# Performance work log

Measured on AMD Instinct MI355X. Metric: run time of the kernel, lower is better.

Reference implementation:

```python
import jax, jax.numpy as jnp
import numpy as np

B, T, L_CTX = 64, 150, 256
H = 512   # decoder_num_hidden
E = 512   # target_embedding_size
V = 1000  # target_vocab_size


def setup_inputs() -> dict:
    key = jax.random.key(0)
    ks = jax.random.split(key, 10)
    s = 0.05
    return {
        "cnn_feats": jax.random.normal(ks[0], (B, L_CTX, H), dtype=jnp.float32),
        "seq": jax.random.randint(ks[1], (B, T), 0, V, dtype=jnp.int32),
        "embed_table": jax.random.normal(ks[2], (V, E), dtype=jnp.float32) * s,
        "W_ih": jax.random.normal(ks[3], (4 * H, E), dtype=jnp.float32) * s,
        "b_ih": jnp.zeros((4 * H,), dtype=jnp.float32),
        "W_hh": jax.random.normal(ks[4], (4 * H, H), dtype=jnp.float32) * s,
        "b_hh": jnp.zeros((4 * H,), dtype=jnp.float32),
        "W_hm": jax.random.normal(ks[5], (H, H), dtype=jnp.float32) * s,
        "W_om": jax.random.normal(ks[6], (H, 2 * H), dtype=jnp.float32) * s,
        "W_logit": jax.random.normal(ks[7], (V, H), dtype=jnp.float32) * s,
        "b_logit": jnp.zeros((V,), dtype=jnp.float32),
    }


def reference(cnn_feats, seq, embed_table, W_ih, b_ih, W_hh, b_hh,
              W_hm, W_om, W_logit, b_logit):
    # Single-layer LSTMCell decoder with per-step attention (eval mode, dropout=0).
    def step(carry, it):
        h, c = carry                      # [B,H] each
        xt = jax.nn.relu(embed_table[it])  # [B,E]
        gates = xt @ W_ih.T + b_ih + h @ W_hh.T + b_hh  # [B,4H]
        i, f, g, o = jnp.split(gates, 4, axis=1)
        c2 = jax.nn.sigmoid(f) * c + jax.nn.sigmoid(i) * jnp.tanh(g)
        h2 = jax.nn.sigmoid(o) * jnp.tanh(c2)
        mapped = h2 @ W_hm.T              # [B,H]
        attn = jnp.einsum("blh,bh->bl", cnn_feats, mapped)
        w = jax.nn.softmax(attn, axis=1)
        ctx = jnp.einsum("bl,blh->bh", w, cnn_feats)
        out = jnp.concatenate([ctx, h2], axis=1) @ W_om.T  # [B,H]
        logp = jax.nn.log_softmax(out @ W_logit.T + b_logit, axis=1)
        return (h2, c2), logp

    bsz = cnn_feats.shape[0]
    h0 = jnp.zeros((bsz, W_hh.shape[1]), dtype=cnn_feats.dtype)
    c0 = jnp.zeros_like(h0)
    _, outs = jax.lax.scan(step, (h0, c0), seq.T)  # outs: [T,B,V]
    return outs.transpose(1, 0, 2)  # [B,T,V]
```

## Files before the change

kernel.cpp:

```cpp
#include <hip/hip_runtime.h>
#include <math.h>

#define B_  64
#define T_  150
#define L_  256
#define H_  512
#define E_  512
#define V_  1000
#define G4_ 2048
#define DB_ 16
#define HCB 32

typedef _Float16 f16;
typedef f16   f16x8 __attribute__((ext_vector_type(8)));
typedef f16   f16x4 __attribute__((ext_vector_type(4)));
typedef float f32x4 __attribute__((ext_vector_type(4)));
typedef unsigned long long ull;

__device__ __forceinline__ float sigmf(float x) { return 1.0f / (1.0f + expf(-x)); }

__global__ __launch_bounds__(512) void decoder_mfma(
    const int*   __restrict__ seq,
    const float* __restrict__ G,
    const float* __restrict__ Whh,
    ull*  __restrict__ xh,
    int*  __restrict__ tags,
    float* __restrict__ hbuf)
{
    __shared__ f16   hlds[64][520];
    __shared__ float glds[64][132];
    __shared__ float csh[64][36];

    const int tid = threadIdx.x;
    const int bb  = blockIdx.x;
    const int ln  = tid & 63;
    const int wv  = tid >> 6;
    const int mh  = wv >> 2;
    const int nt2 = wv & 3;

    f16x8 bfr[2][16];
    #pragma unroll
    for (int j = 0; j < 2; ++j) {
        const int n = 2 * nt2 + j;
        const int grow = (n >> 1) * H_ + bb * HCB + (n & 1) * 16 + (ln & 15);
        #pragma unroll
        for (int kt = 0; kt < 16; ++kt) {
            const int k0 = kt * 32 + (ln >> 4) * 8;
            float4 w0 = *(const float4*)(Whh + (size_t)grow * H_ + k0);
            float4 w1 = *(const float4*)(Whh + (size_t)grow * H_ + k0 + 4);
            bfr[j][kt] = (f16x8){(f16)w0.x, (f16)w0.y, (f16)w0.z, (f16)w0.w,
                                 (f16)w1.x, (f16)w1.y, (f16)w1.z, (f16)w1.w};
        }
    }
    for (int e = tid; e < 64 * 520 / 4; e += 512) ((ull*)hlds)[e] = 0ull;
    for (int e = tid; e < 64 * 36; e += 512) ((float*)csh)[e] = 0.f;
    __syncthreads();

    const int cb = tid >> 3, cg = tid & 7;

    for (int t = 0; t < T_; ++t) {
        const int v = seq[cb * T_ + t];
        const float* gp = G + (size_t)v * G4_ + bb * HCB + cg * 4;
        float4 gq0 = *(const float4*)(gp);
        float4 gq1 = *(const float4*)(gp + H_);
        float4 gq2 = *(const float4*)(gp + 2 * H_);
        float4 gq3 = *(const float4*)(gp + 3 * H_);

        if (t > 0) {
            if (tid < DB_) {
                while (__hip_atomic_load(&tags[tid], __ATOMIC_RELAXED,
                                         __HIP_MEMORY_SCOPE_AGENT) < t) {}
            }
            __syncthreads();
            const ull* src = xh + (size_t)(t & 1) * 64 * 128;
            ull v0[8], v1[8];
            #pragma unroll
            for (int it = 0; it < 8; ++it) {
                const int e = tid + it * 512;
                const int b = e >> 6, s = e & 63;
                v0[it] = __hip_atomic_load(&src[b * 128 + 2 * s], __ATOMIC_RELAXED,
                                           __HIP_MEMORY_SCOPE_AGENT);
                v1[it] = __hip_atomic_load(&src[b * 128 + 2 * s + 1], __ATOMIC_RELAXED,
                                           __HIP_MEMORY_SCOPE_AGENT);
            }
            #pragma unroll
            for (int it = 0; it < 8; ++it) {
                const int e = tid + it * 512;
                const int b = e >> 6, s = e & 63;
                ull* dst = (ull*)&hlds[b][s * 8];
                dst[0] = v0[it]; dst[1] = v1[it];
            }
            __syncthreads();
        }

        f32x4 acc00 = {0.f,0.f,0.f,0.f}, acc01 = {0.f,0.f,0.f,0.f};
        f32x4 acc10 = {0.f,0.f,0.f,0.f}, acc11 = {0.f,0.f,0.f,0.f};
        #pragma unroll
        for (int kt = 0; kt < 16; ++kt) {
            const int ko = kt * 32 + (ln >> 4) * 8;
            f16x8 a0 = *(const f16x8*)&hlds[(2 * mh)     * 16 + (ln & 15)][ko];
            f16x8 a1 = *(const f16x8*)&hlds[(2 * mh + 1) * 16 + (ln & 15)][ko];
            acc00 = __builtin_amdgcn_mfma_f32_16x16x32_f16(a0, bfr[0][kt], acc00, 0, 0, 0);
            acc01 = __builtin_amdgcn_mfma_f32_16x16x32_f16(a0, bfr[1][kt], acc01, 0, 0, 0);
            acc10 = __builtin_amdgcn_mfma_f32_16x16x32_f16(a1, bfr[0][kt], acc10, 0, 0, 0);
            acc11 = __builtin_amdgcn_mfma_f32_16x16x32_f16(a1, bfr[1][kt], acc11, 0, 0, 0);
        }
        {
            const int r0 = (2 * mh) * 16 + (ln >> 4) * 4;
            const int r1 = (2 * mh + 1) * 16 + (ln >> 4) * 4;
            const int c0 = (2 * nt2) * 16 + (ln & 15);
            const int c1 = (2 * nt2 + 1) * 16 + (ln & 15);
            #pragma unroll
            for (int i = 0; i < 4; ++i) {
                glds[r0 + i][c0] = acc00[i];
                glds[r0 + i][c1] = acc01[i];
                glds[r1 + i][c0] = acc10[i];
                glds[r1 + i][c1] = acc11[i];
            }
        }
        __syncthreads();

        {
            float4 Gi = *(const float4*)&glds[cb][cg * 4];
            float4 Gf = *(const float4*)&glds[cb][32 + cg * 4];
            float4 Gg = *(const float4*)&glds[cb][64 + cg * 4];
            float4 Go = *(const float4*)&glds[cb][96 + cg * 4];
            float4 cold = *(const float4*)&csh[cb][cg * 4];
            float gi[4] = {Gi.x + gq0.x, Gi.y + gq0.y, Gi.z + gq0.z, Gi.w + gq0.w};
            float gf[4] = {Gf.x + gq1.x, Gf.y + gq1.y, Gf.z + gq1.z, Gf.w + gq1.w};
            float gg[4] = {Gg.x + gq2.x, Gg.y + gq2.y, Gg.z + gq2.z, Gg.w + gq2.w};
            float go[4] = {Go.x + gq3.x, Go.y + gq3.y, Go.z + gq3.z, Go.w + gq3.w};
            float cl[4] = {cold.x, cold.y, cold.z, cold.w};
            float4 cnew, hnew;
            f16x4 hp;
            #pragma unroll
            for (int i = 0; i < 4; ++i) {
                float c2 = sigmf(gf[i]) * cl[i] + sigmf(gi[i]) * tanhf(gg[i]);
                float h2 = sigmf(go[i]) * tanhf(c2);
                ((float*)&cnew)[i] = c2;
                ((float*)&hnew)[i] = h2;
                hp[i] = (f16)h2;
            }
            *(float4*)&csh[cb][cg * 4] = cnew;
            *(float4*)&hbuf[((size_t)t * 64 + cb) * H_ + bb * HCB + cg * 4] = hnew;
            __hip_atomic_store(
                &xh[(size_t)((t + 1) & 1) * 64 * 128 + cb * 128 + bb * 8 + cg],
                __builtin_bit_cast(ull, hp),
                __ATOMIC_RELAXED, __HIP_MEMORY_SCOPE_AGENT);
        }
        __syncthreads();
        if (tid == 0)
            __hip_atomic_store(&tags[bb], t + 1, __ATOMIC_RELAXED,
                               __HIP_MEMORY_SCOPE_AGENT);
    }
}

template<bool RELU_A, bool REMAP>
__global__ __launch_bounds__(256) void gemm16_nt(
    const float* __restrict__ A1, const float* __restrict__ A2,
    const float* __restrict__ Bm,
    const float* __restrict__ bias1, const float* __restrict__ bias2,
    float* __restrict__ C, int M, int N, int KA)
{
    __shared__ f16 As[64][40];
    __shared__ f16 Bs[64][40];
    const int tid = threadIdx.x;
    const int m0 = blockIdx.x * 64, n0 = blockIdx.y * 64;
    const int ln = tid & 63, wv = tid >> 6;
    const int lr = tid >> 2, lc8 = (tid & 3) * 8;
    const int K = A2 ? 2 * KA : KA;
    f32x4 acc[4] = {};

    for (int kb = 0; kb < K; kb += 32) {
        const float* Ap; int kk;
        if (kb < KA) { Ap = A1; kk = kb; } else { Ap = A2; kk = kb - KA; }
        int gm = m0 + lr;
        float4 a0 = make_float4(0.f, 0.f, 0.f, 0.f), a1 = a0;
        if (gm < M) {
            a0 = *(const float4*)(Ap + (size_t)gm * KA + kk + lc8);
            a1 = *(const float4*)(Ap + (size_t)gm * KA + kk + lc8 + 4);
        }
        if (RELU_A) {
            a0.x = fmaxf(a0.x, 0.f); a0.y = fmaxf(a0.y, 0.f);
            a0.z = fmaxf(a0.z, 0.f); a0.w = fmaxf(a0.w, 0.f);
            a1.x = fmaxf(a1.x, 0.f); a1.y = fmaxf(a1.y, 0.f);
            a1.z = fmaxf(a1.z, 0.f); a1.w = fmaxf(a1.w, 0.f);
        }
        f16x8 av = {(f16)a0.x, (f16)a0.y, (f16)a0.z, (f16)a0.w,
                    (f16)a1.x, (f16)a1.y, (f16)a1.z, (f16)a1.w};
        *(f16x8*)&As[lr][lc8] = av;

        int gn = n0 + lr;
        float4 b0 = make_float4(0.f, 0.f, 0.f, 0.f), b1 = b0;
        if (gn < N) {
            b0 = *(const float4*)(Bm + (size_t)gn * K + kb + lc8);
            b1 = *(const float4*)(Bm + (size_t)gn * K + kb + lc8 + 4);
        }
        f16x8 bv = {(f16)b0.x, (f16)b0.y, (f16)b0.z, (f16)b0.w,
                    (f16)b1.x, (f16)b1.y, (f16)b1.z, (f16)b1.w};
        *(f16x8*)&Bs[lr][lc8] = bv;
        __syncthreads();

        f16x8 af = *(const f16x8*)&As[wv * 16 + (ln & 15)][(ln >> 4) * 8];
        #pragma unroll
        for (int ntt = 0; ntt < 4; ++ntt) {
            f16x8 bf = *(const f16x8*)&Bs[ntt * 16 + (ln & 15)][(ln >> 4) * 8];
            acc[ntt] = __builtin_amdgcn_mfma_f32_16x16x32_f16(af, bf, acc[ntt], 0, 0, 0);
        }
        __syncthreads();
    }

    #pragma unroll
    for (int ntt = 0; ntt < 4; ++ntt) {
        #pragma unroll
        for (int i = 0; i < 4; ++i) {
            int gm = m0 + wv * 16 + (ln >> 4) * 4 + i;
            int gn = n0 + ntt * 16 + (ln & 15);
            if (gm < M && gn < N) {
                float v = acc[ntt][i];
                if (bias1) v += bias1[gn];
                if (bias2) v += bias2[gn];
                size_t row = REMAP ? ((size_t)(gm & 63) * T_ + (gm >> 6)) : (size_t)gm;
                C[row * (size_t)N + gn] = v;
            }
        }
    }
}

__global__ __launch_bounds__(256) void gemm_nt(
    const float* __restrict__ A, size_t lda, size_t azs,
    const float* __restrict__ Bm, size_t ldb, size_t bzs,
    float* __restrict__ C, size_t ldc, size_t czs, int M, int N, int K)
{
    A  += blockIdx.z * azs;
    Bm += blockIdx.z * bzs;
    C  += blockIdx.z * czs;
    __shared__ __align__(16) float As[16][68];
    __shared__ __align__(16) float Bs[16][68];
    const int tid = threadIdx.x;
    const int m0 = blockIdx.x * 64;
    const int n0 = blockIdx.y * 64;
    const int lr = tid >> 2;
    const int lc = (tid & 3) << 2;
    const int tm = (tid & 15) << 2;
    const int tn = (tid >> 4) << 2;
    float acc[4][4] = {};

    for (int kb = 0; kb < K; kb += 16) {
        float4 a4 = make_float4(0.f, 0.f, 0.f, 0.f);
        int gm = m0 + lr;
        if (gm < M) a4 = *(const float4*)(A + (size_t)gm * lda + kb + lc);
        As[lc + 0][lr] = a4.x; As[lc + 1][lr] = a4.y;
        As[lc + 2][lr] = a4.z; As[lc + 3][lr] = a4.w;

        float4 b4 = make_float4(0.f, 0.f, 0.f, 0.f);
        int gn = n0 + lr;
        if (gn < N) b4 = *(const float4*)(Bm + (size_t)gn * ldb + kb + lc);
        Bs[lc + 0][lr] = b4.x; Bs[lc + 1][lr] = b4.y;
        Bs[lc + 2][lr] = b4.z; Bs[lc + 3][lr] = b4.w;
        __syncthreads();

        #pragma unroll
        for (int k = 0; k < 16; ++k) {
            float4 av = *(const float4*)&As[k][tm];
            float4 bv = *(const float4*)&Bs[k][tn];
            float af[4] = {av.x, av.y, av.z, av.w};
            float bf[4] = {bv.x, bv.y, bv.z, bv.w};
            #pragma unroll
            for (int i = 0; i < 4; ++i)
                #pragma unroll
                for (int j = 0; j < 4; ++j)
                    acc[i][j] += af[i] * bf[j];
        }
        __syncthreads();
    }

    #pragma unroll
    for (int i = 0; i < 4; ++i) {
        int gm = m0 + tm + i;
        if (gm >= M) continue;
        #pragma unroll
        for (int j = 0; j < 4; ++j) {
            int gn = n0 + tn + j;
            if (gn >= N) continue;
            C[(size_t)gm * ldc + gn] = acc[i][j];
        }
    }
}

__global__ __launch_bounds__(256) void gemm_nn(
    const float* __restrict__ A, size_t lda, size_t azs,
    const float* __restrict__ Bm, size_t ldb, size_t bzs,
    float* __restrict__ C, size_t ldc, size_t czs, int M, int N, int K)
{
    A  += blockIdx.z * azs;
    Bm += blockIdx.z * bzs;
    C  += blockIdx.z * czs;
    __shared__ __align__(16) float As[16][68];
    __shared__ __align__(16) float Bs[16][68];
    const int tid = threadIdx.x;
    const int m0 = blockIdx.x * 64;
    const int n0 = blockIdx.y * 64;
    const int lr = tid >> 2;
    const int lc = (tid & 3) << 2;
    const int br = tid >> 4;
    const int bc = (tid & 15) << 2;
    const int tm = (tid & 15) << 2;
    const int tn = (tid >> 4) << 2;
    float acc[4][4] = {};

    for (int kb = 0; kb < K; kb += 16) {
        float4 a4 = make_float4(0.f, 0.f, 0.f, 0.f);
        int gm = m0 + lr;
        if (gm < M) a4 = *(const float4*)(A + (size_t)gm * lda + kb + lc);
        As[lc + 0][lr] = a4.x; As[lc + 1][lr] = a4.y;
        As[lc + 2][lr] = a4.z; As[lc + 3][lr] = a4.w;

        float4 b4 = make_float4(0.f, 0.f, 0.f, 0.f);
        if (n0 + bc < N) b4 = *(const float4*)(Bm + (size_t)(kb + br) * ldb + n0 + bc);
        Bs[br][bc + 0] = b4.x; Bs[br][bc + 1] = b4.y;
        Bs[br][bc + 2] = b4.z; Bs[br][bc + 3] = b4.w;
        __syncthreads();

        #pragma unroll
        for (int k = 0; k < 16; ++k) {
            float4 av = *(const float4*)&As[k][tm];
            float4 bv = *(const float4*)&Bs[k][tn];
            float af[4] = {av.x, av.y, av.z, av.w};
            float bf[4] = {bv.x, bv.y, bv.z, bv.w};
            #pragma unroll
            for (int i = 0; i < 4; ++i)
                #pragma unroll
                for (int j = 0; j < 4; ++j)
                    acc[i][j] += af[i] * bf[j];
        }
        __syncthreads();
    }

    #pragma unroll
    for (int i = 0; i < 4; ++i) {
        int gm = m0 + tm + i;
        if (gm >= M) continue;
        #pragma unroll
        for (int j = 0; j < 4; ++j) {
            int gn = n0 + tn + j;
            if (gn >= N) continue;
            C[(size_t)gm * ldc + gn] = acc[i][j];
        }
    }
}

__global__ __launch_bounds__(256) void att_softmax(float* __restrict__ att, int nrows)
{
    const int tid = threadIdx.x, lane = tid & 63, wave = tid >> 6;
    const int row = blockIdx.x * 4 + wave;
    if (row >= nrows) return;
    float4* p = (float4*)(att + (size_t)row * L_);
    float4 sc = p[lane];
    float mx = fmaxf(fmaxf(sc.x, sc.y), fmaxf(sc.z, sc.w));
    #pragma unroll
    for (int off = 32; off; off >>= 1) mx = fmaxf(mx, __shfl_xor(mx, off));
    float e0 = expf(sc.x - mx), e1 = expf(sc.y - mx);
    float e2 = expf(sc.z - mx), e3 = expf(sc.w - mx);
    float s = e0 + e1 + e2 + e3;
    #pragma unroll
    for (int off = 32; off; off >>= 1) s += __shfl_xor(s, off);
    float inv = 1.f / s;
    p[lane] = make_float4(e0 * inv, e1 * inv, e2 * inv, e3 * inv);
}

__global__ __launch_bounds__(256) void logsoftmax_k(float* __restrict__ out)
{
    const int row = blockIdx.x;
    float* p = out + (size_t)row * V_;
    const int tid = threadIdx.x, lane = tid & 63, wave = tid >> 6;
    __shared__ float red[8];

    float vals[4];
    int n = 0;
    float mx = -INFINITY;
    for (int v = tid; v < V_; v += 256) { vals[n] = p[v]; mx = fmaxf(mx, vals[n]); ++n; }
    #pragma unroll
    for (int off = 32; off; off >>= 1) mx = fmaxf(mx, __shfl_xor(mx, off));
    if (lane == 0) red[wave] = mx;
    __syncthreads();
    mx = fmaxf(fmaxf(red[0], red[1]), fmaxf(red[2], red[3]));

    float s = 0.f;
    for (int i = 0; i < n; ++i) s += expf(vals[i] - mx);
    #pragma unroll
    for (int off = 32; off; off >>= 1) s += __shfl_xor(s, off);
    if (lane == 0) red[4 + wave] = s;
    __syncthreads();
    s = red[4] + red[5] + red[6] + red[7];

    const float lse = mx + logf(s);
    n = 0;
    for (int v = tid; v < V_; v += 256) { p[v] = vals[n] - lse; ++n; }
}

extern "C" void kernel_launch(void* const* d_in, const int* in_sizes, int n_in,
                              void* d_out, int out_size, void* d_ws, size_t ws_size,
                              hipStream_t stream)
{
    const float* cnn     = (const float*)d_in[0];
    const int*   seq     = (const int*)d_in[1];
    const float* embed   = (const float*)d_in[2];
    const float* W_ih    = (const float*)d_in[3];
    const float* b_ih    = (const float*)d_in[4];
    const float* W_hh    = (const float*)d_in[5];
    const float* b_hh    = (const float*)d_in[6];
    const float* W_hm    = (const float*)d_in[7];
    const float* W_om    = (const float*)d_in[8];
    const float* W_logit = (const float*)d_in[9];
    const float* b_logit = (const float*)d_in[10];
    float* out = (float*)d_out;

    float* ws = (float*)d_ws;
    float* G    = ws;
    float* hbuf = G + (size_t)V_ * G4_;
    float* outv = hbuf + (size_t)B_ * T_ * H_;
    ull*   xh   = (ull*)(outv + (size_t)B_ * T_ * H_);
    int*   tags = (int*)(xh + 2 * 64 * 128);
    float* mapped = out;
    float* attb   = out + (size_t)B_ * T_ * H_;

    hipMemsetAsync(tags, 0, DB_ * sizeof(int), stream);

    gemm16_nt<true, false><<<dim3(16, 32), 256, 0, stream>>>(
        embed, nullptr, W_ih, b_ih, b_hh, G, V_, G4_, E_);

    decoder_mfma<<<DB_, 512, 0, stream>>>(seq, G, W_hh, xh, tags, hbuf);

    gemm16_nt<false, false><<<dim3(150, 8), 256, 0, stream>>>(
        hbuf, nullptr, W_hm, nullptr, nullptr, mapped, B_ * T_, H_, H_);
    gemm_nt<<<dim3(3, 4, 64), 256, 0, stream>>>(
        mapped, (size_t)B_ * H_, H_,
        cnn, H_, (size_t)L_ * H_,
        attb, L_, (size_t)T_ * L_, T_, L_, H_);
    att_softmax<<<(B_ * T_ + 3) / 4, 256, 0, stream>>>(attb, B_ * T_);
    gemm_nn<<<dim3(3, 8, 64), 256, 0, stream>>>(
        attb, L_, (size_t)T_ * L_,
        cnn, H_, (size_t)L_ * H_,
        mapped, (size_t)B_ * H_, H_, T_, H_, L_);
    gemm16_nt<false, false><<<dim3(150, 8), 256, 0, stream>>>(
        mapped, hbuf, W_om, nullptr, nullptr, outv, B_ * T_, H_, H_);
    gemm16_nt<false, true><<<dim3(150, 16), 256, 0, stream>>>(
        outv, nullptr, W_logit, b_logit, nullptr, out, B_ * T_, V_, H_);
    logsoftmax_k<<<B_ * T_, 256, 0, stream>>>(out);
}
```

Measured before the change: 1.078 ms.

## Fuse attention and output head into decoder kernel with consumer blocks overlapping recurrence

Launches 64 extra consumer blocks alongside the 16 recurrence blocks. Each consumer block waits on the per-step tags, reads 16 steps of h history for its batch row and computes the mapping, attention scores, softmax, context, output projection, logits and log-softmax in fp16 MFMA. This overlaps the post-recurrence work with the sequential LSTM and removes several separate GEMM and softmax launches along with the fp32 intermediate buffers. It adds pre-cast fp16 weight and transposed-feature kernels plus a full h history buffer, and it depends on all 80 blocks being co-resident to avoid deadlock.

```diff
diff --git a/kernel.cpp b/kernel.cpp
--- a/kernel.cpp
+++ b/kernel.cpp
@@ -19,60 +19,68 @@
 
 __device__ __forceinline__ float sigmf(float x) { return 1.0f / (1.0f + expf(-x)); }
 
-__global__ __launch_bounds__(512) void decoder_mfma(
+__global__ __launch_bounds__(512) void fused_decoder(
     const int*   __restrict__ seq,
     const float* __restrict__ G,
     const float* __restrict__ Whh,
-    ull*  __restrict__ xh,
+    const float* __restrict__ cnn,
+    const f16*   __restrict__ Vt16,
+    const f16*   __restrict__ Whm16,
+    const f16*   __restrict__ Wom16,
+    const f16*   __restrict__ Wlogit16,
+    const float* __restrict__ b_logit,
+    ull*  __restrict__ xhist,
     int*  __restrict__ tags,
-    float* __restrict__ hbuf)
+    float* __restrict__ out)
 {
-    __shared__ f16   hlds[64][520];
-    __shared__ float glds[64][132];
-    __shared__ float csh[64][36];
+    __shared__ __align__(16) char smem[140800];
 
     const int tid = threadIdx.x;
-    const int bb  = blockIdx.x;
+    const int bx  = blockIdx.x;
     const int ln  = tid & 63;
     const int wv  = tid >> 6;
-    const int mh  = wv >> 2;
-    const int nt2 = wv & 3;
-
-    f16x8 bfr[2][16];
-    #pragma unroll
-    for (int j = 0; j < 2; ++j) {
-        const int n = 2 * nt2 + j;
-        const int grow = (n >> 1) * H_ + bb * HCB + (n & 1) * 16 + (ln & 15);
+
+    if (bx < DB_) {
+        f16   (*hlds)[520] = (f16(*)[520])smem;
+        float (*glds)[132] = (float(*)[132])(smem + 66560);
+        float (*csh)[36]   = (float(*)[36])(smem + 100352);
+        const int bb  = bx;
+        const int mh  = wv >> 2;
+        const int nt2 = wv & 3;
+
+        f16x8 bfr[2][16];
         #pragma unroll
-        for (int kt = 0; kt < 16; ++kt) {
-            const int k0 = kt * 32 + (ln >> 4) * 8;
-            float4 w0 = *(const float4*)(Whh + (size_t)grow * H_ + k0);
-            float4 w1 = *(const float4*)(Whh + (size_t)grow * H_ + k0 + 4);
-            bfr[j][kt] = (f16x8){(f16)w0.x, (f16)w0.y, (f16)w0.z, (f16)w0.w,
-                                 (f16)w1.x, (f16)w1.y, (f16)w1.z, (f16)w1.w};
-        }
-    }
-    for (int e = tid; e < 64 * 520 / 4; e += 512) ((ull*)hlds)[e] = 0ull;
-    for (int e = tid; e < 64 * 36; e += 512) ((float*)csh)[e] = 0.f;
-    __syncthreads();
-
-    const int cb = tid >> 3, cg = tid & 7;
-
-    for (int t = 0; t < T_; ++t) {
-        const int v = seq[cb * T_ + t];
-        const float* gp = G + (size_t)v * G4_ + bb * HCB + cg * 4;
-        float4 gq0 = *(const float4*)(gp);
-        float4 gq1 = *(const float4*)(gp + H_);
-        float4 gq2 = *(const float4*)(gp + 2 * H_);
-        float4 gq3 = *(const float4*)(gp + 3 * H_);
-
-        if (t > 0) {
+        for (int j = 0; j < 2; ++j) {
+            const int n = 2 * nt2 + j;
+            const int grow = (n >> 1) * H_ + bb * HCB + (n & 1) * 16 + (ln & 15);
+            #pragma unroll
+            for (int kt = 0; kt < 16; ++kt) {
+                const int k0 = kt * 32 + (ln >> 4) * 8;
+                float4 w0 = *(const float4*)(Whh + (size_t)grow * H_ + k0);
+                float4 w1 = *(const float4*)(Whh + (size_t)grow * H_ + k0 + 4);
+                bfr[j][kt] = (f16x8){(f16)w0.x, (f16)w0.y, (f16)w0.z, (f16)w0.w,
+                                     (f16)w1.x, (f16)w1.y, (f16)w1.z, (f16)w1.w};
+            }
+        }
+        for (int e = tid; e < 64 * 36; e += 512) ((float*)csh)[e] = 0.f;
+        __syncthreads();
+
+        const int cb = tid >> 3, cg = tid & 7;
+
+        for (int t = 0; t < T_; ++t) {
+            const int v = seq[cb * T_ + t];
+            const float* gp = G + (size_t)v * G4_ + bb * HCB + cg * 4;
+            float4 gq0 = *(const float4*)(gp);
+            float4 gq1 = *(const float4*)(gp + H_);
+            float4 gq2 = *(const float4*)(gp + 2 * H_);
+            float4 gq3 = *(const float4*)(gp + 3 * H_);
+
             if (tid < DB_) {
                 while (__hip_atomic_load(&tags[tid], __ATOMIC_RELAXED,
                                          __HIP_MEMORY_SCOPE_AGENT) < t) {}
             }
             __syncthreads();
-            const ull* src = xh + (size_t)(t & 1) * 64 * 128;
+            const ull* src = xhist + (size_t)t * 8192;
             ull v0[8], v1[8];
             #pragma unroll
             for (int it = 0; it < 8; ++it) {
@@ -91,76 +99,240 @@
                 dst[0] = v0[it]; dst[1] = v1[it];
             }
             __syncthreads();
-        }
-
-        f32x4 acc00 = {0.f,0.f,0.f,0.f}, acc01 = {0.f,0.f,0.f,0.f};
-        f32x4 acc10 = {0.f,0.f,0.f,0.f}, acc11 = {0.f,0.f,0.f,0.f};
-        #pragma unroll
-        for (int kt = 0; kt < 16; ++kt) {
-            const int ko = kt * 32 + (ln >> 4) * 8;
-            f16x8 a0 = *(const f16x8*)&hlds[(2 * mh)     * 16 + (ln & 15)][ko];
-            f16x8 a1 = *(const f16x8*)&hlds[(2 * mh + 1) * 16 + (ln & 15)][ko];
-            acc00 = __builtin_amdgcn_mfma_f32_16x16x32_f16(a0, bfr[0][kt], acc00, 0, 0, 0);
-            acc01 = __builtin_amdgcn_mfma_f32_16x16x32_f16(a0, bfr[1][kt], acc01, 0, 0, 0);
-            acc10 = __builtin_amdgcn_mfma_f32_16x16x32_f16(a1, bfr[0][kt], acc10, 0, 0, 0);
-            acc11 = __builtin_amdgcn_mfma_f32_16x16x32_f16(a1, bfr[1][kt], acc11, 0, 0, 0);
-        }
-        {
-            const int r0 = (2 * mh) * 16 + (ln >> 4) * 4;
-            const int r1 = (2 * mh + 1) * 16 + (ln >> 4) * 4;
-            const int c0 = (2 * nt2) * 16 + (ln & 15);
-            const int c1 = (2 * nt2 + 1) * 16 + (ln & 15);
-            #pragma unroll
-            for (int i = 0; i < 4; ++i) {
-                glds[r0 + i][c0] = acc00[i];
-                glds[r0 + i][c1] = acc01[i];
-                glds[r1 + i][c0] = acc10[i];
-                glds[r1 + i][c1] = acc11[i];
-            }
-        }
-        __syncthreads();
-
-        {
-            float4 Gi = *(const float4*)&glds[cb][cg * 4];
-            float4 Gf = *(const float4*)&glds[cb][32 + cg * 4];
-            float4 Gg = *(const float4*)&glds[cb][64 + cg * 4];
-            float4 Go = *(const float4*)&glds[cb][96 + cg * 4];
-            float4 cold = *(const float4*)&csh[cb][cg * 4];
-            float gi[4] = {Gi.x + gq0.x, Gi.y + gq0.y, Gi.z + gq0.z, Gi.w + gq0.w};
-            float gf[4] = {Gf.x + gq1.x, Gf.y + gq1.y, Gf.z + gq1.z, Gf.w + gq1.w};
-            float gg[4] = {Gg.x + gq2.x, Gg.y + gq2.y, Gg.z + gq2.z, Gg.w + gq2.w};
-            float go[4] = {Go.x + gq3.x, Go.y + gq3.y, Go.z + gq3.z, Go.w + gq3.w};
-            float cl[4] = {cold.x, cold.y, cold.z, cold.w};
-            float4 cnew, hnew;
-            f16x4 hp;
-            #pragma unroll
-            for (int i = 0; i < 4; ++i) {
-                float c2 = sigmf(gf[i]) * cl[i] + sigmf(gi[i]) * tanhf(gg[i]);
-                float h2 = sigmf(go[i]) * tanhf(c2);
-                ((float*)&cnew)[i] = c2;
-                ((float*)&hnew)[i] = h2;
-                hp[i] = (f16)h2;
-            }
-            *(float4*)&csh[cb][cg * 4] = cnew;
-            *(float4*)&hbuf[((size_t)t * 64 + cb) * H_ + bb * HCB + cg * 4] = hnew;
-            __hip_atomic_store(
-                &xh[(size_t)((t + 1) & 1) * 64 * 128 + cb * 128 + bb * 8 + cg],
-                __builtin_bit_cast(ull, hp),
-                __ATOMIC_RELAXED, __HIP_MEMORY_SCOPE_AGENT);
-        }
-        __syncthreads();
-        if (tid == 0)
-            __hip_atomic_store(&tags[bb], t + 1, __ATOMIC_RELAXED,
-                               __HIP_MEMORY_SCOPE_AGENT);
+
+            f32x4 acc00 = {0.f,0.f,0.f,0.f}, acc01 = {0.f,0.f,0.f,0.f};
+            f32x4 acc10 = {0.f,0.f,0.f,0.f}, acc11 = {0.f,0.f,0.f,0.f};
+            #pragma unroll
+            for (int kt = 0; kt < 16; ++kt) {
+                const int ko = kt * 32 + (ln >> 4) * 8;
+                f16x8 a0 = *(const f16x8*)&hlds[(2 * mh)     * 16 + (ln & 15)][ko];
+                f16x8 a1 = *(const f16x8*)&hlds[(2 * mh + 1) * 16 + (ln & 15)][ko];
+                acc00 = __builtin_amdgcn_mfma_f32_16x16x32_f16(a0, bfr[0][kt], acc00, 0, 0, 0);
+                acc01 = __builtin_amdgcn_mfma_f32_16x16x32_f16(a0, bfr[1][kt], acc01, 0, 0, 0);
+                acc10 = __builtin_amdgcn_mfma_f32_16x16x32_f16(a1, bfr[0][kt], acc10, 0, 0, 0);
+                acc11 = __builtin_amdgcn_mfma_f32_16x16x32_f16(a1, bfr[1][kt], acc11, 0, 0, 0);
+            }
+            {
+                const int r0 = (2 * mh) * 16 + (ln >> 4) * 4;
+                const int r1 = (2 * mh + 1) * 16 + (ln >> 4) * 4;
+                const int c0 = (2 * nt2) * 16 + (ln & 15);
+                const int c1 = (2 * nt2 + 1) * 16 + (ln & 15);
+                #pragma unroll
+                for (int i = 0; i < 4; ++i) {
+                    glds[r0 + i][c0] = acc00[i];
+                    glds[r0 + i][c1] = acc01[i];
+                    glds[r1 + i][c0] = acc10[i];
+                    glds[r1 + i][c1] = acc11[i];
+                }
+            }
+            __syncthreads();
+
+            {
+                float4 Gi = *(const float4*)&glds[cb][cg * 4];
+                float4 Gf = *(const float4*)&glds[cb][32 + cg * 4];
+                float4 Gg = *(const float4*)&glds[cb][64 + cg * 4];
+                float4 Go = *(const float4*)&glds[cb][96 + cg * 4];
+                float4 cold = *(const float4*)&csh[cb][cg * 4];
+                float gi[4] = {Gi.x + gq0.x, Gi.y + gq0.y, Gi.z + gq0.z, Gi.w + gq0.w};
+                float gf[4] = {Gf.x + gq1.x, Gf.y + gq1.y, Gf.z + gq1.z, Gf.w + gq1.w};
+                float gg[4] = {Gg.x + gq2.x, Gg.y + gq2.y, Gg.z + gq2.z, Gg.w + gq2.w};
+                float go[4] = {Go.x + gq3.x, Go.y + gq3.y, Go.z + gq3.z, Go.w + gq3.w};
+                float cl[4] = {cold.x, cold.y, cold.z, cold.w};
+                float4 cnew;
+                f16x4 hp;
+                #pragma unroll
+                for (int i = 0; i < 4; ++i) {
+                    float c2 = sigmf(gf[i]) * cl[i] + sigmf(gi[i]) * tanhf(gg[i]);
+                    float h2 = sigmf(go[i]) * tanhf(c2);
+                    ((float*)&cnew)[i] = c2;
+                    hp[i] = (f16)h2;
+                }
+                *(float4*)&csh[cb][cg * 4] = cnew;
+                __hip_atomic_store(
+                    &xhist[(size_t)(t + 1) * 8192 + cb * 128 + bb * 8 + cg],
+                    __builtin_bit_cast(ull, hp),
+                    __ATOMIC_RELAXED, __HIP_MEMORY_SCOPE_AGENT);
+            }
+            __syncthreads();
+            if (tid == 0)
+                __hip_atomic_store(&tags[bb], t + 1, __ATOMIC_RELAXED,
+                                   __HIP_MEMORY_SCOPE_AGENT);
+        }
+    } else {
+        const int b = bx - DB_;
+        f16   (*hl)[520]  = (f16(*)[520])smem;
+        f16   (*ml)[520]  = (f16(*)[520])(smem + 16640);
+        float (*sl)[260]  = (float(*)[260])(smem + 33280);
+        f16   (*pl)[264]  = (f16(*)[264])(smem + 49920);
+        f16   (*ol)[520]  = (f16(*)[520])(smem + 58368);
+        float (*ll)[1028] = (float(*)[1028])(smem + 75008);
+
+        const float* cnnb = cnn + (size_t)b * L_ * H_;
+        const f16*   vtb  = Vt16 + (size_t)b * H_ * L_;
+        const int ln15 = ln & 15;
+        const int ln4  = (ln >> 4) * 8;
+        const int lr4  = (ln >> 4) * 4;
+
+        for (int t0 = 0; t0 < T_; t0 += 16) {
+            const int NB = (T_ - t0 < 16) ? (T_ - t0) : 16;
+            if (tid < DB_) {
+                while (__hip_atomic_load(&tags[tid], __ATOMIC_RELAXED,
+                                         __HIP_MEMORY_SCOPE_AGENT) < t0 + NB)
+                    __builtin_amdgcn_s_sleep(8);
+            }
+            __syncthreads();
+            for (int e = tid; e < NB * 128; e += 512) {
+                int tt = e >> 7, s = e & 127;
+                ull v = __hip_atomic_load(
+                    &xhist[(size_t)(t0 + 1 + tt) * 8192 + b * 128 + s],
+                    __ATOMIC_RELAXED, __HIP_MEMORY_SCOPE_AGENT);
+                *(ull*)&hl[tt][s * 4] = v;
+            }
+            __syncthreads();
+
+            {
+                f32x4 acc[4] = {};
+                for (int kt = 0; kt < 16; ++kt) {
+                    f16x8 a = *(const f16x8*)&hl[ln15][kt * 32 + ln4];
+                    #pragma unroll
+                    for (int j = 0; j < 4; ++j) {
+                        int n = wv * 64 + j * 16 + ln15;
+                        f16x8 bf = *(const f16x8*)(Whm16 + (size_t)n * 512 + kt * 32 + ln4);
+                        acc[j] = __builtin_amdgcn_mfma_f32_16x16x32_f16(a, bf, acc[j], 0, 0, 0);
+                    }
+                }
+                #pragma unroll
+                for (int j = 0; j < 4; ++j)
+                    #pragma unroll
+                    for (int i = 0; i < 4; ++i)
+                        ml[lr4 + i][wv * 64 + j * 16 + ln15] = (f16)acc[j][i];
+            }
+            __syncthreads();
+            {
+                f32x4 acc[2] = {};
+                for (int kt = 0; kt < 16; ++kt) {
+                    f16x8 a = *(const f16x8*)&ml[ln15][kt * 32 + ln4];
+                    #pragma unroll
+                    for (int j = 0; j < 2; ++j) {
+                        int l = wv * 32 + j * 16 + ln15;
+                        float4 w0 = *(const float4*)(cnnb + (size_t)l * H_ + kt * 32 + ln4);
+                        float4 w1 = *(const float4*)(cnnb + (size_t)l * H_ + kt * 32 + ln4 + 4);
+                        f16x8 bf = {(f16)w0.x, (f16)w0.y, (f16)w0.z, (f16)w0.w,
+                                    (f16)w1.x, (f16)w1.y, (f16)w1.z, (f16)w1.w};
+                        acc[j] = __builtin_amdgcn_mfma_f32_16x16x32_f16(a, bf, acc[j], 0, 0, 0);
+                    }
+                }
+                #pragma unroll
+                for (int j = 0; j < 2; ++j)
+                    #pragma unroll
+                    for (int i = 0; i < 4; ++i)
+                        sl[lr4 + i][wv * 32 + j * 16 + ln15] = acc[j][i];
+            }
+            __syncthreads();
+            #pragma unroll
+            for (int rr = 0; rr < 2; ++rr) {
+                int r = wv * 2 + rr;
+                float4 v = *(const float4*)&sl[r][ln * 4];
+                float mx = fmaxf(fmaxf(v.x, v.y), fmaxf(v.z, v.w));
+                #pragma unroll
+                for (int off = 32; off; off >>= 1) mx = fmaxf(mx, __shfl_xor(mx, off));
+                float e0 = expf(v.x - mx), e1 = expf(v.y - mx);
+                float e2 = expf(v.z - mx), e3 = expf(v.w - mx);
+                float s = e0 + e1 + e2 + e3;
+                #pragma unroll
+                for (int off = 32; off; off >>= 1) s += __shfl_xor(s, off);
+                float inv = 1.f / s;
+                f16x4 p = {(f16)(e0 * inv), (f16)(e1 * inv), (f16)(e2 * inv), (f16)(e3 * inv)};
+                *(f16x4*)&pl[r][ln * 4] = p;
+            }
+            __syncthreads();
+            {
+                f32x4 acc[4] = {};
+                for (int kt = 0; kt < 8; ++kt) {
+                    f16x8 a = *(const f16x8*)&pl[ln15][kt * 32 + ln4];
+                    #pragma unroll
+                    for (int j = 0; j < 4; ++j) {
+                        int n = wv * 64 + j * 16 + ln15;
+                        f16x8 bf = *(const f16x8*)(vtb + (size_t)n * L_ + kt * 32 + ln4);
+                        acc[j] = __builtin_amdgcn_mfma_f32_16x16x32_f16(a, bf, acc[j], 0, 0, 0);
+                    }
+                }
+                __syncthreads();
+                #pragma unroll
+                for (int j = 0; j < 4; ++j)
+                    #pragma unroll
+                    for (int i = 0; i < 4; ++i)
+                        ml[lr4 + i][wv * 64 + j * 16 + ln15] = (f16)acc[j][i];
+            }
+            __syncthreads();
+            {
+                f32x4 acc[4] = {};
+                for (int kt = 0; kt < 32; ++kt) {
+                    f16x8 a = (kt < 16)
+                        ? *(const f16x8*)&ml[ln15][kt * 32 + ln4]
+                        : *(const f16x8*)&hl[ln15][(kt - 16) * 32 + ln4];
+                    #pragma unroll
+                    for (int j = 0; j < 4; ++j) {
+                        int n = wv * 64 + j * 16 + ln15;
+                        f16x8 bf = *(const f16x8*)(Wom16 + (size_t)n * 1024 + kt * 32 + ln4);
+                        acc[j] = __builtin_amdgcn_mfma_f32_16x16x32_f16(a, bf, acc[j], 0, 0, 0);
+                    }
+                }
+                #pragma unroll
+                for (int j = 0; j < 4; ++j)
+                    #pragma unroll
+                    for (int i = 0; i < 4; ++i)
+                        ol[lr4 + i][wv * 64 + j * 16 + ln15] = (f16)acc[j][i];
+            }
+            __syncthreads();
+            {
+                f32x4 acc[8] = {};
+                for (int kt = 0; kt < 16; ++kt) {
+                    f16x8 a = *(const f16x8*)&ol[ln15][kt * 32 + ln4];
+                    #pragma unroll
+                    for (int j = 0; j < 8; ++j) {
+                        int n = wv * 128 + j * 16 + ln15;
+                        f16x8 bf = *(const f16x8*)(Wlogit16 + (size_t)n * 512 + kt * 32 + ln4);
+                        acc[j] = __builtin_amdgcn_mfma_f32_16x16x32_f16(a, bf, acc[j], 0, 0, 0);
+                    }
+                }
+                #pragma unroll
+                for (int j = 0; j < 8; ++j) {
+                    int n = wv * 128 + j * 16 + ln15;
+                    float bias = (n < V_) ? b_logit[n] : 0.f;
+                    #pragma unroll
+                    for (int i = 0; i < 4; ++i)
+                        ll[lr4 + i][n] = acc[j][i] + bias;
+                }
+            }
+            __syncthreads();
+            #pragma unroll
+            for (int rr = 0; rr < 2; ++rr) {
+                int r = wv * 2 + rr;
+                if (r < NB) {
+                    float mx = -INFINITY;
+                    for (int i = ln; i < V_; i += 64) mx = fmaxf(mx, ll[r][i]);
+                    #pragma unroll
+                    for (int off = 32; off; off >>= 1) mx = fmaxf(mx, __shfl_xor(mx, off));
+                    float s = 0.f;
+                    for (int i = ln; i < V_; i += 64) s += expf(ll[r][i] - mx);
+                    #pragma unroll
+                    for (int off = 32; off; off >>= 1) s += __shfl_xor(s, off);
+                    float lse = mx + logf(s);
+                    float* dst = out + ((size_t)b * T_ + t0 + r) * V_;
+                    for (int i = ln; i < V_; i += 64) dst[i] = ll[r][i] - lse;
+                }
+            }
+            __syncthreads();
+        }
     }
 }
 
-template<bool RELU_A, bool REMAP>
+template<bool RELU_A>
 __global__ __launch_bounds__(256) void gemm16_nt(
-    const float* __restrict__ A1, const float* __restrict__ A2,
-    const float* __restrict__ Bm,
+    const float* __restrict__ A1, const float* __restrict__ Bm,
     const float* __restrict__ bias1, const float* __restrict__ bias2,
-    float* __restrict__ C, int M, int N, int KA)
+    float* __restrict__ C, int M, int N, int K)
 {
     __shared__ f16 As[64][40];
     __shared__ f16 Bs[64][40];
@@ -168,17 +340,14 @@
     const int m0 = blockIdx.x * 64, n0 = blockIdx.y * 64;
     const int ln = tid & 63, wv = tid >> 6;
     const int lr = tid >> 2, lc8 = (tid & 3) * 8;
-    const int K = A2 ? 2 * KA : KA;
     f32x4 acc[4] = {};
 
     for (int kb = 0; kb < K; kb += 32) {
-        const float* Ap; int kk;
-        if (kb < KA) { Ap = A1; kk = kb; } else { Ap = A2; kk = kb - KA; }
         int gm = m0 + lr;
         float4 a0 = make_float4(0.f, 0.f, 0.f, 0.f), a1 = a0;
         if (gm < M) {
-            a0 = *(const float4*)(Ap + (size_t)gm * KA + kk + lc8);
-            a1 = *(const float4*)(Ap + (size_t)gm * KA + kk + lc8 + 4);
+            a0 = *(const float4*)(A1 + (size_t)gm * K + kb + lc8);
+            a1 = *(const float4*)(A1 + (size_t)gm * K + kb + lc8 + 4);
         }
         if (RELU_A) {
             a0.x = fmaxf(a0.x, 0.f); a0.y = fmaxf(a0.y, 0.f);
@@ -211,7 +380,7 @@
     }
 
     #pragma unroll
-    for (int ntt = 0; ntt < 4; ++ntt) {
+    for (int ntt = 0; ntt < 4; ++ntt)
         #pragma unroll
         for (int i = 0; i < 4; ++i) {
             int gm = m0 + wv * 16 + (ln >> 4) * 4 + i;
@@ -220,183 +389,36 @@
                 float v = acc[ntt][i];
                 if (bias1) v += bias1[gn];
                 if (bias2) v += bias2[gn];
-                size_t row = REMAP ? ((size_t)(gm & 63) * T_ + (gm >> 6)) : (size_t)gm;
-                C[row * (size_t)N + gn] = v;
-            }
-        }
-    }
+                C[(size_t)gm * N + gn] = v;
+            }
+        }
 }
 
-__global__ __launch_bounds__(256) void gemm_nt(
-    const float* __restrict__ A, size_t lda, size_t azs,
-    const float* __restrict__ Bm, size_t ldb, size_t bzs,
-    float* __restrict__ C, size_t ldc, size_t czs, int M, int N, int K)
+__global__ __launch_bounds__(256) void wcast(
+    const float* __restrict__ whm, const float* __restrict__ wom,
+    const float* __restrict__ wlg,
+    f16* __restrict__ o_whm, f16* __restrict__ o_wom, f16* __restrict__ o_wlg)
 {
-    A  += blockIdx.z * azs;
-    Bm += blockIdx.z * bzs;
-    C  += blockIdx.z * czs;
-    __shared__ __align__(16) float As[16][68];
-    __shared__ __align__(16) float Bs[16][68];
-    const int tid = threadIdx.x;
-    const int m0 = blockIdx.x * 64;
-    const int n0 = blockIdx.y * 64;
-    const int lr = tid >> 2;
-    const int lc = (tid & 3) << 2;
-    const int tm = (tid & 15) << 2;
-    const int tn = (tid >> 4) << 2;
-    float acc[4][4] = {};
-
-    for (int kb = 0; kb < K; kb += 16) {
-        float4 a4 = make_float4(0.f, 0.f, 0.f, 0.f);
-        int gm = m0 + lr;
-        if (gm < M) a4 = *(const float4*)(A + (size_t)gm * lda + kb + lc);
-        As[lc + 0][lr] = a4.x; As[lc + 1][lr] = a4.y;
-        As[lc + 2][lr] = a4.z; As[lc + 3][lr] = a4.w;
-
-        float4 b4 = make_float4(0.f, 0.f, 0.f, 0.f);
-        int gn = n0 + lr;
-        if (gn < N) b4 = *(const float4*)(Bm + (size_t)gn * ldb + kb + lc);
-        Bs[lc + 0][lr] = b4.x; Bs[lc + 1][lr] = b4.y;
-        Bs[lc + 2][lr] = b4.z; Bs[lc + 3][lr] = b4.w;
-        __syncthreads();
-
-        #pragma unroll
-        for (int k = 0; k < 16; ++k) {
-            float4 av = *(const float4*)&As[k][tm];
-            float4 bv = *(const float4*)&Bs[k][tn];
-            float af[4] = {av.x, av.y, av.z, av.w};
-            float bf[4] = {bv.x, bv.y, bv.z, bv.w};
-            #pragma unroll
-            for (int i = 0; i < 4; ++i)
-                #pragma unroll
-                for (int j = 0; j < 4; ++j)
-                    acc[i][j] += af[i] * bf[j];
-        }
-        __syncthreads();
-    }
-
-    #pragma unroll
-    for (int i = 0; i < 4; ++i) {
-        int gm = m0 + tm + i;
-        if (gm >= M) continue;
-        #pragma unroll
-        for (int j = 0; j < 4; ++j) {
-            int gn = n0 + tn + j;
-            if (gn >= N) continue;
-            C[(size_t)gm * ldc + gn] = acc[i][j];
-        }
-    }
+    const int stride = gridDim.x * 256;
+    for (int i = blockIdx.x * 256 + threadIdx.x; i < 262144; i += stride)
+        o_whm[i] = (f16)whm[i];
+    for (int i = blockIdx.x * 256 + threadIdx.x; i < 524288; i += stride)
+        o_wom[i] = (f16)wom[i];
+    for (int i = blockIdx.x * 256 + threadIdx.x; i < 524288; i += stride)
+        o_wlg[i] = (i < 512000) ? (f16)wlg[i] : (f16)0.f;
 }
 
-__global__ __launch_bounds__(256) void gemm_nn(
-    const float* __restrict__ A, size_t lda, size_t azs,
-    const float* __restrict__ Bm, size_t ldb, size_t bzs,
-    float* __restrict__ C, size_t ldc, size_t czs, int M, int N, int K)
+__global__ __launch_bounds__(256) void vtrans(
+    const float* __restrict__ cnn, f16* __restrict__ Vt16)
 {
-    A  += blockIdx.z * azs;
-    Bm += blockIdx.z * bzs;
-    C  += blockIdx.z * czs;
-    __shared__ __align__(16) float As[16][68];
-    __shared__ __align__(16) float Bs[16][68];
-    const int tid = threadIdx.x;
-    const int m0 = blockIdx.x * 64;
-    const int n0 = blockIdx.y * 64;
-    const int lr = tid >> 2;
-    const int lc = (tid & 3) << 2;
-    const int br = tid >> 4;
-    const int bc = (tid & 15) << 2;
-    const int tm = (tid & 15) << 2;
-    const int tn = (tid >> 4) << 2;
-    float acc[4][4] = {};
-
-    for (int kb = 0; kb < K; kb += 16) {
-        float4 a4 = make_float4(0.f, 0.f, 0.f, 0.f);
-        int gm = m0 + lr;
-        if (gm < M) a4 = *(const float4*)(A + (size_t)gm * lda + kb + lc);
-        As[lc + 0][lr] = a4.x; As[lc + 1][lr] = a4.y;
-        As[lc + 2][lr] = a4.z; As[lc + 3][lr] = a4.w;
-
-        float4 b4 = make_float4(0.f, 0.f, 0.f, 0.f);
-        if (n0 + bc < N) b4 = *(const float4*)(Bm + (size_t)(kb + br) * ldb + n0 + bc);
-        Bs[br][bc + 0] = b4.x; Bs[br][bc + 1] = b4.y;
-        Bs[br][bc + 2] = b4.z; Bs[br][bc + 3] = b4.w;
-        __syncthreads();
-
-        #pragma unroll
-        for (int k = 0; k < 16; ++k) {
-            float4 av = *(const float4*)&As[k][tm];
-            float4 bv = *(const float4*)&Bs[k][tn];
-            float af[4] = {av.x, av.y, av.z, av.w};
-            float bf[4] = {bv.x, bv.y, bv.z, bv.w};
-            #pragma unroll
-            for (int i = 0; i < 4; ++i)
-                #pragma unroll
-                for (int j = 0; j < 4; ++j)
-                    acc[i][j] += af[i] * bf[j];
-        }
-        __syncthreads();
-    }
-
-    #pragma unroll
-    for (int i = 0; i < 4; ++i) {
-        int gm = m0 + tm + i;
-        if (gm >= M) continue;
-        #pragma unroll
-        for (int j = 0; j < 4; ++j) {
-            int gn = n0 + tn + j;
-            if (gn >= N) continue;
-            C[(size_t)gm * ldc + gn] = acc[i][j];
-        }
-    }
-}
-
-__global__ __launch_bounds__(256) void att_softmax(float* __restrict__ att, int nrows)
-{
-    const int tid = threadIdx.x, lane = tid & 63, wave = tid >> 6;
-    const int row = blockIdx.x * 4 + wave;
-    if (row >= nrows) return;
-    float4* p = (float4*)(att + (size_t)row * L_);
-    float4 sc = p[lane];
-    float mx = fmaxf(fmaxf(sc.x, sc.y), fmaxf(sc.z, sc.w));
-    #pragma unroll
-    for (int off = 32; off; off >>= 1) mx = fmaxf(mx, __shfl_xor(mx, off));
-    float e0 = expf(sc.x - mx), e1 = expf(sc.y - mx);
-    float e2 = expf(sc.z - mx), e3 = expf(sc.w - mx);
-    float s = e0 + e1 + e2 + e3;
-    #pragma unroll
-    for (int off = 32; off; off >>= 1) s += __shfl_xor(s, off);
-    float inv = 1.f / s;
-    p[lane] = make_float4(e0 * inv, e1 * inv, e2 * inv, e3 * inv);
-}
-
-__global__ __launch_bounds__(256) void logsoftmax_k(float* __restrict__ out)
-{
-    const int row = blockIdx.x;
-    float* p = out + (size_t)row * V_;
-    const int tid = threadIdx.x, lane = tid & 63, wave = tid >> 6;
-    __shared__ float red[8];
-
-    float vals[4];
-    int n = 0;
-    float mx = -INFINITY;
-    for (int v = tid; v < V_; v += 256) { vals[n] = p[v]; mx = fmaxf(mx, vals[n]); ++n; }
-    #pragma unroll
-    for (int off = 32; off; off >>= 1) mx = fmaxf(mx, __shfl_xor(mx, off));
-    if (lane == 0) red[wave] = mx;
+    __shared__ f16 tile[32][34];
+    const int j0 = blockIdx.x * 32, l0 = blockIdx.y * 32, b = blockIdx.z;
+    const int x = threadIdx.x & 31, y = threadIdx.x >> 5;
+    for (int i = y; i < 32; i += 8)
+        tile[i][x] = (f16)cnn[((size_t)b * L_ + l0 + i) * H_ + j0 + x];
     __syncthreads();
-    mx = fmaxf(fmaxf(red[0], red[1]), fmaxf(red[2], red[3]));
-
-    float s = 0.f;
-    for (int i = 0; i < n; ++i) s += expf(vals[i] - mx);
-    #pragma unroll
-    for (int off = 32; off; off >>= 1) s += __shfl_xor(s, off);
-    if (lane == 0) red[4 + wave] = s;
-    __syncthreads();
-    s = red[4] + red[5] + red[6] + red[7];
-
-    const float lse = mx + logf(s);
-    n = 0;
-    for (int v = tid; v < V_; v += 256) { p[v] = vals[n] - lse; ++n; }
+    for (int i = y; i < 32; i += 8)
+        Vt16[((size_t)b * H_ + j0 + i) * L_ + l0 + x] = tile[x][i];
 }
 
 extern "C" void kernel_launch(void* const* d_in, const int* in_sizes, int n_in,
@@ -416,36 +438,24 @@
     const float* b_logit = (const float*)d_in[10];
     float* out = (float*)d_out;
 
-    float* ws = (float*)d_ws;
-    float* G    = ws;
-    float* hbuf = G + (size_t)V_ * G4_;
-    float* outv = hbuf + (size_t)B_ * T_ * H_;
-    ull*   xh   = (ull*)(outv + (size_t)B_ * T_ * H_);
-    int*   tags = (int*)(xh + 2 * 64 * 128);
-    float* mapped = out;
-    float* attb   = out + (size_t)B_ * T_ * H_;
+    char* ws = (char*)d_ws;
+    float* G        = (float*)ws;
+    ull*   xhist    = (ull*)(ws + 8192000);
+    f16*   Vt16     = (f16*)(ws + 8192000 + 9904128);
+    f16*   Whm16    = (f16*)(ws + 34873344);
+    f16*   Wom16    = (f16*)(ws + 35397632);
+    f16*   Wlogit16 = (f16*)(ws + 36446208);
+    int*   tags     = (int*)(ws + 37494784);
 
     hipMemsetAsync(tags, 0, DB_ * sizeof(int), stream);
-
-    gemm16_nt<true, false><<<dim3(16, 32), 256, 0, stream>>>(
-        embed, nullptr, W_ih, b_ih, b_hh, G, V_, G4_, E_);
-
-    decoder_mfma<<<DB_, 512, 0, stream>>>(seq, G, W_hh, xh, tags, hbuf);
-
-    gemm16_nt<false, false><<<dim3(150, 8), 256, 0, stream>>>(
-        hbuf, nullptr, W_hm, nullptr, nullptr, mapped, B_ * T_, H_, H_);
-    gemm_nt<<<dim3(3, 4, 64), 256, 0, stream>>>(
-        mapped, (size_t)B_ * H_, H_,
-        cnn, H_, (size_t)L_ * H_,
-        attb, L_, (size_t)T_ * L_, T_, L_, H_);
-    att_softmax<<<(B_ * T_ + 3) / 4, 256, 0, stream>>>(attb, B_ * T_);
-    gemm_nn<<<dim3(3, 8, 64), 256, 0, stream>>>(
-        attb, L_, (size_t)T_ * L_,
-        cnn, H_, (size_t)L_ * H_,
-        mapped, (size_t)B_ * H_, H_, T_, H_, L_);
-    gemm16_nt<false, false><<<dim3(150, 8), 256, 0, stream>>>(
-        mapped, hbuf, W_om, nullptr, nullptr, outv, B_ * T_, H_, H_);
-    gemm16_nt<false, true><<<dim3(150, 16), 256, 0, stream>>>(
-        outv, nullptr, W_logit, b_logit, nullptr, out, B_ * T_, V_, H_);
-    logsoftmax_k<<<B_ * T_, 256, 0, stream>>>(out);
+    hipMemsetAsync(xhist, 0, 8192 * sizeof(ull), stream);
+
+    gemm16_nt<true><<<dim3(16, 32), 256, 0, stream>>>(
+        embed, W_ih, b_ih, b_hh, G, V_, G4_, E_);
+    wcast<<<512, 256, 0, stream>>>(W_hm, W_om, W_logit, Whm16, Wom16, Wlogit16);
+    vtrans<<<dim3(16, 8, 64), 256, 0, stream>>>(cnn, Vt16);
+
+    fused_decoder<<<DB_ + B_, 512, 0, stream>>>(
+        seq, G, W_hh, cnn, Vt16, Whm16, Wom16, Wlogit16, b_logit,
+        xhist, tags, out);
 }
```

Result: slower. 1.567 ms (+45.4%).
